# Optimization experiments

Measured on AMD Instinct MI355X. Metric: run time of the kernel, lower is better.

Reference implementation:

```python
import jax, jax.numpy as jnp
import numpy as np

IN_CH = 128
HID = 256   # 2 * out_channels
OUT_CH = 128
N_NODES = 10000
N_EDGES = 640000


def setup_inputs() -> dict:
    key = jax.random.key(0)
    ks = jax.random.split(key, 6)
    x = jax.random.normal(ks[0], (N_NODES, IN_CH), dtype=jnp.float32)
    edge_index = jax.random.randint(ks[1], (2, N_EDGES), 0, N_NODES, dtype=jnp.int64)
    # GCNConv params (glorot-like scale)
    W1 = jax.random.normal(ks[2], (IN_CH, HID), dtype=jnp.float32) / np.sqrt(IN_CH)
    b1 = jnp.zeros((HID,), dtype=jnp.float32)
    W2 = jax.random.normal(ks[3], (HID, OUT_CH), dtype=jnp.float32) / np.sqrt(HID)
    b2 = jnp.zeros((OUT_CH,), dtype=jnp.float32)
    return {"x": x, "edge_index": edge_index, "W1": W1, "b1": b1, "W2": W2, "b2": b2}


def _gcn_norm(edge_index, n_nodes):
    """Add self-loops and compute symmetric GCN normalization per edge."""
    loops = jnp.arange(n_nodes, dtype=edge_index.dtype)
    src = jnp.concatenate([edge_index[0], loops])  # [E+N]
    dst = jnp.concatenate([edge_index[1], loops])
    deg = jax.ops.segment_sum(jnp.ones_like(dst, dtype=jnp.float32), dst,
                              num_segments=n_nodes)
    dinv = jnp.where(deg > 0, jax.lax.rsqrt(deg), 0.0)
    norm = dinv[src] * dinv[dst]  # [E+N]
    return src, dst, norm


def _gcn_layer(x, W, b, src, dst, norm, n_nodes):
    h = x @ W                                  # [N, F_out]
    msg = h[src] * norm[:, None]               # gather + scale, [E+N, F_out]
    agg = jax.ops.segment_sum(msg, dst, num_segments=n_nodes)
    return agg + b


def reference(x, edge_index, W1, b1, W2, b2):
    n = x.shape[0]
    src, dst, norm = _gcn_norm(edge_index, n)
    h = jax.nn.relu(_gcn_layer(x, W1, b1, src, dst, norm, n))
    out = jax.nn.relu(_gcn_layer(h, W2, b2, src, dst, norm, n))
    return out
```

## Files before the change

kernel.cpp:

```cpp
#include <hip/hip_runtime.h>

#define N_FEAT 128
#define HID 256
#define OUT_CH 128

#define NB 256
#define MAXN 10240
#define CH 16
#define CB (NB / CH)

__device__ __forceinline__ unsigned bf16rn(float f) {
    unsigned u = __float_as_uint(f);
    return (u + 0x7fffu + ((u >> 16) & 1u)) >> 16;
}
__device__ __forceinline__ unsigned pack_bf16x2(float lo, float hi) {
    return bf16rn(lo) | (bf16rn(hi) << 16);
}
__device__ __forceinline__ float2 unpack_bf16x2(unsigned u) {
    float2 r;
    r.x = __uint_as_float(u << 16);
    r.y = __uint_as_float(u & 0xffff0000u);
    return r;
}


__global__ __launch_bounds__(256)
void hist_kernel(const int* __restrict__ dst, unsigned short* __restrict__ bh,
                 int E, int N, int chunk) {
    __shared__ int hist[MAXN];
    for (int i = threadIdx.x; i < N; i += 256) hist[i] = 0;
    __syncthreads();
    int base = blockIdx.x * chunk;
    int lim = min(chunk, E - base);
    for (int i = threadIdx.x; i < lim; i += 256) {
        int d = dst[base + i];
        if (d >= 0 && d < N) atomicAdd(&hist[d], 1);
    }
    __syncthreads();
    unsigned short* out = bh + (size_t)blockIdx.x * N;
    for (int i = threadIdx.x; i < N; i += 256) out[i] = (unsigned short)hist[i];
}

__global__ __launch_bounds__(256)
void colscan_kernel(const unsigned short* __restrict__ bh,
                    int* __restrict__ ps, int* __restrict__ counts,
                    float* __restrict__ dinv, int N) {
    int j = blockIdx.x * 256 + threadIdx.x;
    if (j >= N) return;
    int run = 0;
    for (int c = 0; c < CH; c++) {
        int s = 0;
        #pragma unroll
        for (int b = c * CB; b < (c + 1) * CB; b++) s += bh[(size_t)b * N + j];
        ps[(size_t)c * N + j] = run;
        run += s;
    }
    counts[j] = run;
    dinv[j] = rsqrtf((float)(run + 1));
}

#define SCAN_T 1024
#define SCAN_MAX_PER 16
__global__ __launch_bounds__(SCAN_T)
void scan_kernel(const int* __restrict__ counts,
                 int* __restrict__ row_start, int n) {
    int tid = threadIdx.x;
    int per = (n + SCAN_T - 1) / SCAN_T;
    int base = tid * per;
    int local[SCAN_MAX_PER];
    int sum = 0;
    for (int j = 0; j < per; j++) {
        int i = base + j;
        int c = (i < n) ? counts[i] : 0;
        local[j] = sum;
        sum += c;
    }
    int lane = tid & 63;
    int wave = tid >> 6;
    int incl = sum;
    #pragma unroll
    for (int off = 1; off < 64; off <<= 1) {
        int t = __shfl_up(incl, off, 64);
        if (lane >= off) incl += t;
    }
    __shared__ int wsum[16];
    __shared__ int woff[16];
    if (lane == 63) wsum[wave] = incl;
    __syncthreads();
    if (wave == 0) {
        int w = (lane < 16) ? wsum[lane] : 0;
        int v = w;
        #pragma unroll
        for (int off = 1; off < 16; off <<= 1) {
            int t = __shfl_up(v, off, 64);
            if (lane >= off) v += t;
        }
        if (lane < 16) woff[lane] = v - w;
    }
    __syncthreads();
    int thread_excl = woff[wave] + (incl - sum);
    for (int j = 0; j < per; j++) {
        int i = base + j;
        if (i < n) row_start[i] = thread_excl + local[j];
    }
    if (tid == SCAN_T - 1) row_start[n] = thread_excl + sum;
}

__global__ __launch_bounds__(256)
void chunkbase_kernel(unsigned short* __restrict__ bh,
                      const int* __restrict__ ps, int N) {
    int j = blockIdx.x * 256 + threadIdx.x;
    if (j >= N) return;
    int c = blockIdx.y;
    int run = ps[(size_t)c * N + j];
    #pragma unroll
    for (int b = c * CB; b < (c + 1) * CB; b++) {
        size_t idx = (size_t)b * N + j;
        int t = bh[idx];
        bh[idx] = (unsigned short)run;
        run += t;
    }
}

__global__ __launch_bounds__(256)
void scat_kernel(const int* __restrict__ src, const int* __restrict__ dst,
                 const unsigned short* __restrict__ bh,
                 const int* __restrict__ row_start,
                 int* __restrict__ csr_src, int E, int N, int chunk) {
    __shared__ int cur[MAXN];
    const unsigned short* basep = bh + (size_t)blockIdx.x * N;
    for (int i = threadIdx.x; i < N; i += 256)
        cur[i] = row_start[i] + (int)basep[i];
    __syncthreads();
    int base = blockIdx.x * chunk;
    int lim = min(chunk, E - base);
    for (int i = threadIdx.x; i < lim; i += 256) {
        int e = base + i;
        int d = dst[e];
        if (d < 0 || d >= N) continue;
        int pos = atomicAdd(&cur[d], 1);
        if ((unsigned)pos < (unsigned)E) csr_src[pos] = src[e];
    }
}

__global__ void prescale_kernel(const float* __restrict__ x,
                                const float* __restrict__ dinv,
                                unsigned* __restrict__ xs_b, int total4) {
    int i = blockIdx.x * blockDim.x + threadIdx.x;
    if (i < total4) {
        int row = i >> 5;
        float d = dinv[row];
        float4 v = ((const float4*)x)[i];
        uint2 p;
        p.x = pack_bf16x2(v.x * d, v.y * d);
        p.y = pack_bf16x2(v.z * d, v.w * d);
        ((uint2*)xs_b)[i] = p;
    }
}

template <bool EPILOGUE>
__global__ __launch_bounds__(256)
void agg_kernel(const unsigned* __restrict__ featb,
                const float* __restrict__ dinv,
                const int* __restrict__ row_start,
                const int* __restrict__ csr_src,
                const float* __restrict__ bias,
                float* __restrict__ out, int N) {
    int wave = threadIdx.x >> 6;
    int n = blockIdx.x * 4 + wave;
    if (n >= N) return;
    int f = threadIdx.x & 63;
    float dn = dinv[n];
    float2 v = unpack_bf16x2(featb[(size_t)n * 64 + f]);
    float accx = v.x;
    float accy = v.y;
    int e0 = row_start[n];
    int e1 = row_start[n + 1];
    int e = e0;
    if (e + 8 <= e1) {
        int s_cur[8];
        #pragma unroll
        for (int j = 0; j < 8; j++) s_cur[j] = csr_src[e + j];
        e += 8;
        for (; e + 8 <= e1; e += 8) {
            unsigned w[8];
            #pragma unroll
            for (int j = 0; j < 8; j++) w[j] = featb[(size_t)s_cur[j] * 64 + f];
            int s_nxt[8];
            #pragma unroll
            for (int j = 0; j < 8; j++) s_nxt[j] = csr_src[e + j];
            #pragma unroll
            for (int j = 0; j < 8; j++) {
                float2 u = unpack_bf16x2(w[j]);
                accx += u.x;
                accy += u.y;
            }
            #pragma unroll
            for (int j = 0; j < 8; j++) s_cur[j] = s_nxt[j];
        }
        unsigned w[8];
        #pragma unroll
        for (int j = 0; j < 8; j++) w[j] = featb[(size_t)s_cur[j] * 64 + f];
        #pragma unroll
        for (int j = 0; j < 8; j++) {
            float2 u = unpack_bf16x2(w[j]);
            accx += u.x;
            accy += u.y;
        }
    }
    for (; e + 4 <= e1; e += 4) {
        int s0 = csr_src[e], s1 = csr_src[e + 1];
        int s2 = csr_src[e + 2], s3 = csr_src[e + 3];
        unsigned w0 = featb[(size_t)s0 * 64 + f];
        unsigned w1 = featb[(size_t)s1 * 64 + f];
        unsigned w2 = featb[(size_t)s2 * 64 + f];
        unsigned w3 = featb[(size_t)s3 * 64 + f];
        float2 u0 = unpack_bf16x2(w0), u1 = unpack_bf16x2(w1);
        float2 u2 = unpack_bf16x2(w2), u3 = unpack_bf16x2(w3);
        accx += u0.x + u1.x + u2.x + u3.x;
        accy += u0.y + u1.y + u2.y + u3.y;
    }
    for (; e < e1; ++e) {
        float2 u = unpack_bf16x2(featb[(size_t)csr_src[e] * 64 + f]);
        accx += u.x;
        accy += u.y;
    }
    accx *= dn;
    accy *= dn;
    if (EPILOGUE) {
        float2 b = ((const float2*)bias)[f];
        accx = fmaxf(accx + b.x, 0.0f);
        accy = fmaxf(accy + b.y, 0.0f);
    }
    float2 r;
    r.x = accx;
    r.y = accy;
    ((float2*)out)[(size_t)n * 64 + f] = r;
}

template <bool BIAS_RELU, bool RSCALE, bool BF16_OUT>
__global__ __launch_bounds__(256)
void gemm_kernel(const float* __restrict__ A,
                 const float* __restrict__ B,
                 const float* __restrict__ bias,
                 const float* __restrict__ rscale,
                 void* __restrict__ Cv, int M, int N, int K) {
    __shared__ float As[16][68];
    __shared__ float Bs[16][64];
    int tid = threadIdx.x;
    int n0 = blockIdx.x * 64;
    int m0 = blockIdx.y * 64;
    int tx = tid & 15;
    int ty = tid >> 4;
    int ar = tid >> 2;
    int akq = tid & 3;
    int bk = tid >> 4;
    int bnq = tid & 15;
    float acc[4][4] = {};
    for (int k0 = 0; k0 < K; k0 += 16) {
        float4 av = make_float4(0.f, 0.f, 0.f, 0.f);
        if (m0 + ar < M)
            av = *(const float4*)&A[(size_t)(m0 + ar) * K + k0 + akq * 4];
        float4 bv = *(const float4*)&B[(size_t)(k0 + bk) * N + n0 + bnq * 4];
        As[akq * 4 + 0][ar] = av.x;
        As[akq * 4 + 1][ar] = av.y;
        As[akq * 4 + 2][ar] = av.z;
        As[akq * 4 + 3][ar] = av.w;
        *(float4*)&Bs[bk][bnq * 4] = bv;
        __syncthreads();
        #pragma unroll
        for (int k = 0; k < 16; k++) {
            float4 ra = *(const float4*)&As[k][ty * 4];
            float4 rb = *(const float4*)&Bs[k][tx * 4];
            acc[0][0] = fmaf(ra.x, rb.x, acc[0][0]);
            acc[0][1] = fmaf(ra.x, rb.y, acc[0][1]);
            acc[0][2] = fmaf(ra.x, rb.z, acc[0][2]);
            acc[0][3] = fmaf(ra.x, rb.w, acc[0][3]);
            acc[1][0] = fmaf(ra.y, rb.x, acc[1][0]);
            acc[1][1] = fmaf(ra.y, rb.y, acc[1][1]);
            acc[1][2] = fmaf(ra.y, rb.z, acc[1][2]);
            acc[1][3] = fmaf(ra.y, rb.w, acc[1][3]);
            acc[2][0] = fmaf(ra.z, rb.x, acc[2][0]);
            acc[2][1] = fmaf(ra.z, rb.y, acc[2][1]);
            acc[2][2] = fmaf(ra.z, rb.z, acc[2][2]);
            acc[2][3] = fmaf(ra.z, rb.w, acc[2][3]);
            acc[3][0] = fmaf(ra.w, rb.x, acc[3][0]);
            acc[3][1] = fmaf(ra.w, rb.y, acc[3][1]);
            acc[3][2] = fmaf(ra.w, rb.z, acc[3][2]);
            acc[3][3] = fmaf(ra.w, rb.w, acc[3][3]);
        }
        __syncthreads();
    }
    #pragma unroll
    for (int i = 0; i < 4; i++) {
        int m = m0 + ty * 4 + i;
        if (m >= M) continue;
        float rs = RSCALE ? rscale[m] : 1.0f;
        float v[4];
        #pragma unroll
        for (int j = 0; j < 4; j++) {
            v[j] = acc[i][j];
            if (RSCALE) v[j] *= rs;
            if (BIAS_RELU) v[j] = fmaxf(v[j] + bias[n0 + tx * 4 + j], 0.0f);
        }
        if (BF16_OUT) {
            unsigned* Cb = (unsigned*)Cv;
            size_t base = (size_t)m * (N >> 1) + ((n0 + tx * 4) >> 1);
            Cb[base] = pack_bf16x2(v[0], v[1]);
            Cb[base + 1] = pack_bf16x2(v[2], v[3]);
        } else {
            float* C = (float*)Cv;
            #pragma unroll
            for (int j = 0; j < 4; j++)
                C[(size_t)m * N + n0 + tx * 4 + j] = v[j];
        }
    }
}


static inline size_t align512(size_t x) { return (x + 511) & ~(size_t)511; }

extern "C" void kernel_launch(void* const* d_in, const int* in_sizes, int n_in,
                              void* d_out, int out_size, void* d_ws, size_t ws_size,
                              hipStream_t stream) {
    const float* x = (const float*)d_in[0];
    const int* ei = (const int*)d_in[1];
    const float* W1 = (const float*)d_in[2];
    const float* b1 = (const float*)d_in[3];
    const float* W2 = (const float*)d_in[4];
    const float* b2 = (const float*)d_in[5];
    float* out = (float*)d_out;

    const int N = in_sizes[0] / N_FEAT;
    const int E = in_sizes[1] / 2;
    const int* src = ei;
    const int* dst = ei + E;

    char* ws = (char*)d_ws;
    size_t off = 0;
    float* dinv = (float*)(ws + off);    off += align512((size_t)N * 4);
    int* counts = (int*)(ws + off);      off += align512((size_t)N * 4);
    int* row_start = (int*)(ws + off);   off += align512((size_t)(N + 1) * 4);
    int* csr_src = (int*)(ws + off);     off += align512((size_t)E * 4);
    unsigned* xs_b = (unsigned*)(ws + off); off += align512((size_t)N * 64 * 4);
    float* h = (float*)(ws + off);       off += align512((size_t)N * HID * 4);
    unsigned* t_b = (unsigned*)(ws + off); off += align512((size_t)N * 64 * 4);
    int* ps = (int*)(ws + off);          off += align512((size_t)CH * N * 4);
    unsigned short* bh = (unsigned short*)(ws + off);
    off += align512((size_t)NB * N * 2);
    (void)ws_size;
    float* agg1 = out;
    const int chunk = (E + NB - 1) / NB;
    const int NJ = (N + 255) / 256;

    hist_kernel<<<NB, 256, 0, stream>>>(dst, bh, E, N, chunk);
    colscan_kernel<<<NJ, 256, 0, stream>>>(bh, ps, counts, dinv, N);
    scan_kernel<<<1, SCAN_T, 0, stream>>>(counts, row_start, N);
    chunkbase_kernel<<<dim3(NJ, CH), 256, 0, stream>>>(bh, ps, N);
    scat_kernel<<<NB, 256, 0, stream>>>(src, dst, bh, row_start, csr_src, E, N, chunk);

    {
        int total4 = N * N_FEAT / 4;
        prescale_kernel<<<(total4 + 255) / 256, 256, 0, stream>>>(x, dinv, xs_b, total4);
    }

    agg_kernel<false><<<(N + 3) / 4, 256, 0, stream>>>(xs_b, dinv, row_start, csr_src,
                                                       nullptr, agg1, N);

    {
        dim3 grid(HID / 64, (N + 63) / 64);
        gemm_kernel<true, false, false><<<grid, 256, 0, stream>>>(
            agg1, W1, b1, nullptr, h, N, HID, N_FEAT);
    }

    {
        dim3 grid(OUT_CH / 64, (N + 63) / 64);
        gemm_kernel<false, true, true><<<grid, 256, 0, stream>>>(
            h, W2, nullptr, dinv, t_b, N, OUT_CH, HID);
    }

    agg_kernel<true><<<(N + 3) / 4, 256, 0, stream>>>(t_b, dinv, row_start, csr_src,
                                                      b2, out, N);
}
```

Measured before the change: 176.5 us.

## Replace FP32 SIMT GEMMs with FP16 MFMA GEMMs and merge CSR prefix passes

Both dense GEMMs move from FP32 FMA tiling to 16x16x32 FP16 MFMA with swizzled LDS tiles. Inputs and intermediates (aggregated features, hidden activations, transformed features) are now stored as FP16 instead of BF16/FP32, and the weights are transposed and converted to FP16 inside the prescale kernel. The two-level per-block histogram scan is folded into one colscan pass that writes exclusive offsets in place, which drops the chunkbase kernel and the ps buffer. The aim is to cut GEMM compute time, intermediate memory traffic and launch count. The cost is FP16 range and precision risk. The GEMM also reads padded rows past N that are never initialised, although those rows are not stored.

```diff
diff --git a/kernel.cpp b/kernel.cpp
--- a/kernel.cpp
+++ b/kernel.cpp
@@ -6,26 +6,31 @@
 
 #define NB 256
 #define MAXN 10240
-#define CH 16
-#define CB (NB / CH)
-
-__device__ __forceinline__ unsigned bf16rn(float f) {
-    unsigned u = __float_as_uint(f);
-    return (u + 0x7fffu + ((u >> 16) & 1u)) >> 16;
-}
-__device__ __forceinline__ unsigned pack_bf16x2(float lo, float hi) {
-    return bf16rn(lo) | (bf16rn(hi) << 16);
-}
-__device__ __forceinline__ float2 unpack_bf16x2(unsigned u) {
-    float2 r;
-    r.x = __uint_as_float(u << 16);
-    r.y = __uint_as_float(u & 0xffff0000u);
-    return r;
-}
-
-
-__global__ __launch_bounds__(256)
-void hist_kernel(const int* __restrict__ dst, unsigned short* __restrict__ bh,
+
+typedef unsigned short u16;
+typedef _Float16 f16x8 __attribute__((ext_vector_type(8)));
+typedef float f32x4 __attribute__((ext_vector_type(4)));
+
+__device__ __forceinline__ unsigned pack_f16x2(float lo, float hi) {
+    union { _Float16 h[2]; unsigned u; } c;
+    c.h[0] = (_Float16)lo;
+    c.h[1] = (_Float16)hi;
+    return c.u;
+}
+__device__ __forceinline__ float2 unpack_f16x2(unsigned u) {
+    union { unsigned u; _Float16 h[2]; } c;
+    c.u = u;
+    return make_float2((float)c.h[0], (float)c.h[1]);
+}
+__device__ __forceinline__ u16 f16u(float f) {
+    union { _Float16 h; u16 u; } c;
+    c.h = (_Float16)f;
+    return c.u;
+}
+
+
+__global__ __launch_bounds__(256)
+void hist_kernel(const int* __restrict__ dst, u16* __restrict__ bh,
                  int E, int N, int chunk) {
     __shared__ int hist[MAXN];
     for (int i = threadIdx.x; i < N; i += 256) hist[i] = 0;
@@ -37,23 +42,22 @@
         if (d >= 0 && d < N) atomicAdd(&hist[d], 1);
     }
     __syncthreads();
-    unsigned short* out = bh + (size_t)blockIdx.x * N;
-    for (int i = threadIdx.x; i < N; i += 256) out[i] = (unsigned short)hist[i];
-}
-
-__global__ __launch_bounds__(256)
-void colscan_kernel(const unsigned short* __restrict__ bh,
-                    int* __restrict__ ps, int* __restrict__ counts,
-                    float* __restrict__ dinv, int N) {
+    u16* out = bh + (size_t)blockIdx.x * N;
+    for (int i = threadIdx.x; i < N; i += 256) out[i] = (u16)hist[i];
+}
+
+__global__ __launch_bounds__(256)
+void colscan_kernel(u16* __restrict__ bh,
+                    int* __restrict__ counts, float* __restrict__ dinv, int N) {
     int j = blockIdx.x * 256 + threadIdx.x;
     if (j >= N) return;
     int run = 0;
-    for (int c = 0; c < CH; c++) {
-        int s = 0;
-        #pragma unroll
-        for (int b = c * CB; b < (c + 1) * CB; b++) s += bh[(size_t)b * N + j];
-        ps[(size_t)c * N + j] = run;
-        run += s;
+    #pragma unroll 8
+    for (int b = 0; b < NB; b++) {
+        size_t idx = (size_t)b * N + j;
+        int t = bh[idx];
+        bh[idx] = (u16)run;
+        run += t;
     }
     counts[j] = run;
     dinv[j] = rsqrtf((float)(run + 1));
@@ -107,28 +111,12 @@
 }
 
 __global__ __launch_bounds__(256)
-void chunkbase_kernel(unsigned short* __restrict__ bh,
-                      const int* __restrict__ ps, int N) {
-    int j = blockIdx.x * 256 + threadIdx.x;
-    if (j >= N) return;
-    int c = blockIdx.y;
-    int run = ps[(size_t)c * N + j];
-    #pragma unroll
-    for (int b = c * CB; b < (c + 1) * CB; b++) {
-        size_t idx = (size_t)b * N + j;
-        int t = bh[idx];
-        bh[idx] = (unsigned short)run;
-        run += t;
-    }
-}
-
-__global__ __launch_bounds__(256)
 void scat_kernel(const int* __restrict__ src, const int* __restrict__ dst,
-                 const unsigned short* __restrict__ bh,
+                 const u16* __restrict__ bh,
                  const int* __restrict__ row_start,
                  int* __restrict__ csr_src, int E, int N, int chunk) {
     __shared__ int cur[MAXN];
-    const unsigned short* basep = bh + (size_t)blockIdx.x * N;
+    const u16* basep = bh + (size_t)blockIdx.x * N;
     for (int i = threadIdx.x; i < N; i += 256)
         cur[i] = row_start[i] + (int)basep[i];
     __syncthreads();
@@ -145,33 +133,49 @@
 
 __global__ void prescale_kernel(const float* __restrict__ x,
                                 const float* __restrict__ dinv,
-                                unsigned* __restrict__ xs_b, int total4) {
+                                unsigned* __restrict__ xs_b,
+                                const float* __restrict__ W1,
+                                const float* __restrict__ W2,
+                                u16* __restrict__ W1t, u16* __restrict__ W2t,
+                                int total4) {
     int i = blockIdx.x * blockDim.x + threadIdx.x;
     if (i < total4) {
         int row = i >> 5;
         float d = dinv[row];
         float4 v = ((const float4*)x)[i];
         uint2 p;
-        p.x = pack_bf16x2(v.x * d, v.y * d);
-        p.y = pack_bf16x2(v.z * d, v.w * d);
+        p.x = pack_f16x2(v.x * d, v.y * d);
+        p.y = pack_f16x2(v.z * d, v.w * d);
         ((uint2*)xs_b)[i] = p;
-    }
-}
-
-template <bool EPILOGUE>
+    } else {
+        int j = i - total4;
+        if (j < N_FEAT * HID) {
+            int n = j >> 7, k = j & 127;
+            W1t[j] = f16u(W1[(size_t)k * HID + n]);
+        } else {
+            j -= N_FEAT * HID;
+            if (j < HID * OUT_CH) {
+                int n = j >> 8, k = j & 255;
+                W2t[j] = f16u(W2[(size_t)k * OUT_CH + n]);
+            }
+        }
+    }
+}
+
+template <bool EPILOGUE, bool F16OUT>
 __global__ __launch_bounds__(256)
 void agg_kernel(const unsigned* __restrict__ featb,
                 const float* __restrict__ dinv,
                 const int* __restrict__ row_start,
                 const int* __restrict__ csr_src,
                 const float* __restrict__ bias,
-                float* __restrict__ out, int N) {
+                void* __restrict__ out, int N) {
     int wave = threadIdx.x >> 6;
     int n = blockIdx.x * 4 + wave;
     if (n >= N) return;
     int f = threadIdx.x & 63;
     float dn = dinv[n];
-    float2 v = unpack_bf16x2(featb[(size_t)n * 64 + f]);
+    float2 v = unpack_f16x2(featb[(size_t)n * 64 + f]);
     float accx = v.x;
     float accy = v.y;
     int e0 = row_start[n];
@@ -191,7 +195,7 @@
             for (int j = 0; j < 8; j++) s_nxt[j] = csr_src[e + j];
             #pragma unroll
             for (int j = 0; j < 8; j++) {
-                float2 u = unpack_bf16x2(w[j]);
+                float2 u = unpack_f16x2(w[j]);
                 accx += u.x;
                 accy += u.y;
             }
@@ -203,7 +207,7 @@
         for (int j = 0; j < 8; j++) w[j] = featb[(size_t)s_cur[j] * 64 + f];
         #pragma unroll
         for (int j = 0; j < 8; j++) {
-            float2 u = unpack_bf16x2(w[j]);
+            float2 u = unpack_f16x2(w[j]);
             accx += u.x;
             accy += u.y;
         }
@@ -215,13 +219,13 @@
         unsigned w1 = featb[(size_t)s1 * 64 + f];
         unsigned w2 = featb[(size_t)s2 * 64 + f];
         unsigned w3 = featb[(size_t)s3 * 64 + f];
-        float2 u0 = unpack_bf16x2(w0), u1 = unpack_bf16x2(w1);
-        float2 u2 = unpack_bf16x2(w2), u3 = unpack_bf16x2(w3);
+        float2 u0 = unpack_f16x2(w0), u1 = unpack_f16x2(w1);
+        float2 u2 = unpack_f16x2(w2), u3 = unpack_f16x2(w3);
         accx += u0.x + u1.x + u2.x + u3.x;
         accy += u0.y + u1.y + u2.y + u3.y;
     }
     for (; e < e1; ++e) {
-        float2 u = unpack_bf16x2(featb[(size_t)csr_src[e] * 64 + f]);
+        float2 u = unpack_f16x2(featb[(size_t)csr_src[e] * 64 + f]);
         accx += u.x;
         accy += u.y;
     }
@@ -232,87 +236,79 @@
         accx = fmaxf(accx + b.x, 0.0f);
         accy = fmaxf(accy + b.y, 0.0f);
     }
-    float2 r;
-    r.x = accx;
-    r.y = accy;
-    ((float2*)out)[(size_t)n * 64 + f] = r;
-}
-
-template <bool BIAS_RELU, bool RSCALE, bool BF16_OUT>
-__global__ __launch_bounds__(256)
-void gemm_kernel(const float* __restrict__ A,
-                 const float* __restrict__ B,
-                 const float* __restrict__ bias,
-                 const float* __restrict__ rscale,
-                 void* __restrict__ Cv, int M, int N, int K) {
-    __shared__ float As[16][68];
-    __shared__ float Bs[16][64];
+    if (F16OUT) {
+        ((unsigned*)out)[(size_t)n * 64 + f] = pack_f16x2(accx, accy);
+    } else {
+        float2 r;
+        r.x = accx;
+        r.y = accy;
+        ((float2*)out)[(size_t)n * 64 + f] = r;
+    }
+}
+
+template <bool BIAS_RELU, bool RSCALE>
+__global__ __launch_bounds__(256)
+void gemm16_kernel(const u16* __restrict__ A,
+                   const u16* __restrict__ Bt,
+                   const float* __restrict__ bias,
+                   const float* __restrict__ rscale,
+                   u16* __restrict__ C,
+                   int M, int N, int K) {
+    __shared__ __align__(16) u16 As[64][64];
+    __shared__ __align__(16) u16 Bs[64][64];
     int tid = threadIdx.x;
+    int w = tid >> 6;
+    int l = tid & 63;
+    int m0 = blockIdx.y * 64;
     int n0 = blockIdx.x * 64;
-    int m0 = blockIdx.y * 64;
-    int tx = tid & 15;
-    int ty = tid >> 4;
-    int ar = tid >> 2;
-    int akq = tid & 3;
-    int bk = tid >> 4;
-    int bnq = tid & 15;
-    float acc[4][4] = {};
-    for (int k0 = 0; k0 < K; k0 += 16) {
-        float4 av = make_float4(0.f, 0.f, 0.f, 0.f);
-        if (m0 + ar < M)
-            av = *(const float4*)&A[(size_t)(m0 + ar) * K + k0 + akq * 4];
-        float4 bv = *(const float4*)&B[(size_t)(k0 + bk) * N + n0 + bnq * 4];
-        As[akq * 4 + 0][ar] = av.x;
-        As[akq * 4 + 1][ar] = av.y;
-        As[akq * 4 + 2][ar] = av.z;
-        As[akq * 4 + 3][ar] = av.w;
-        *(float4*)&Bs[bk][bnq * 4] = bv;
+
+    f32x4 acc[4];
+    const f32x4 zero = {0.f, 0.f, 0.f, 0.f};
+    #pragma unroll
+    for (int n = 0; n < 4; n++) acc[n] = zero;
+
+    int rowA = w * 16 + (l & 15);
+    int cbase = l >> 4;
+
+    for (int k0 = 0; k0 < K; k0 += 64) {
+        #pragma unroll
+        for (int t = 0; t < 2; t++) {
+            int q = tid + t * 256;
+            int r = q >> 3;
+            int c = q & 7;
+            f16x8 av = *(const f16x8*)(A + (size_t)(m0 + r) * K + k0 + c * 8);
+            *(f16x8*)&As[r][(c ^ (r & 7)) * 8] = av;
+            f16x8 bv = *(const f16x8*)(Bt + (size_t)(n0 + r) * K + k0 + c * 8);
+            *(f16x8*)&Bs[r][(c ^ (r & 7)) * 8] = bv;
+        }
         __syncthreads();
         #pragma unroll
-        for (int k = 0; k < 16; k++) {
-            float4 ra = *(const float4*)&As[k][ty * 4];
-            float4 rb = *(const float4*)&Bs[k][tx * 4];
-            acc[0][0] = fmaf(ra.x, rb.x, acc[0][0]);
-            acc[0][1] = fmaf(ra.x, rb.y, acc[0][1]);
-            acc[0][2] = fmaf(ra.x, rb.z, acc[0][2]);
-            acc[0][3] = fmaf(ra.x, rb.w, acc[0][3]);
-            acc[1][0] = fmaf(ra.y, rb.x, acc[1][0]);
-            acc[1][1] = fmaf(ra.y, rb.y, acc[1][1]);
-            acc[1][2] = fmaf(ra.y, rb.z, acc[1][2]);
-            acc[1][3] = fmaf(ra.y, rb.w, acc[1][3]);
-            acc[2][0] = fmaf(ra.z, rb.x, acc[2][0]);
-            acc[2][1] = fmaf(ra.z, rb.y, acc[2][1]);
-            acc[2][2] = fmaf(ra.z, rb.z, acc[2][2]);
-            acc[2][3] = fmaf(ra.z, rb.w, acc[2][3]);
-            acc[3][0] = fmaf(ra.w, rb.x, acc[3][0]);
-            acc[3][1] = fmaf(ra.w, rb.y, acc[3][1]);
-            acc[3][2] = fmaf(ra.w, rb.z, acc[3][2]);
-            acc[3][3] = fmaf(ra.w, rb.w, acc[3][3]);
+        for (int kc = 0; kc < 2; kc++) {
+            int ch = kc * 4 + cbase;
+            f16x8 af = *(const f16x8*)&As[rowA][(ch ^ (rowA & 7)) * 8];
+            #pragma unroll
+            for (int n = 0; n < 4; n++) {
+                int rb = n * 16 + (l & 15);
+                f16x8 bf = *(const f16x8*)&Bs[rb][(ch ^ (rb & 7)) * 8];
+                acc[n] = __builtin_amdgcn_mfma_f32_16x16x32_f16(af, bf, acc[n], 0, 0, 0);
+            }
         }
         __syncthreads();
     }
+    int r0 = (l >> 4) * 2 * 2;
+    int col_l = l & 15;
     #pragma unroll
-    for (int i = 0; i < 4; i++) {
-        int m = m0 + ty * 4 + i;
+    for (int r = 0; r < 4; r++) {
+        int m = m0 + w * 16 + r0 + r;
         if (m >= M) continue;
         float rs = RSCALE ? rscale[m] : 1.0f;
-        float v[4];
-        #pragma unroll
-        for (int j = 0; j < 4; j++) {
-            v[j] = acc[i][j];
-            if (RSCALE) v[j] *= rs;
-            if (BIAS_RELU) v[j] = fmaxf(v[j] + bias[n0 + tx * 4 + j], 0.0f);
-        }
-        if (BF16_OUT) {
-            unsigned* Cb = (unsigned*)Cv;
-            size_t base = (size_t)m * (N >> 1) + ((n0 + tx * 4) >> 1);
-            Cb[base] = pack_bf16x2(v[0], v[1]);
-            Cb[base + 1] = pack_bf16x2(v[2], v[3]);
-        } else {
-            float* C = (float*)Cv;
-            #pragma unroll
-            for (int j = 0; j < 4; j++)
-                C[(size_t)m * N + n0 + tx * 4 + j] = v[j];
+        #pragma unroll
+        for (int n = 0; n < 4; n++) {
+            int col = n0 + n * 16 + col_l;
+            float v = acc[n][r];
+            if (RSCALE) v *= rs;
+            if (BIAS_RELU) v = fmaxf(v + bias[col], 0.0f);
+            C[(size_t)m * N + col] = f16u(v);
         }
     }
 }
@@ -336,49 +332,52 @@
     const int* src = ei;
     const int* dst = ei + E;
 
+    const int Mpad = ((N + 63) / 64) * 64;
+
     char* ws = (char*)d_ws;
     size_t off = 0;
     float* dinv = (float*)(ws + off);    off += align512((size_t)N * 4);
     int* counts = (int*)(ws + off);      off += align512((size_t)N * 4);
     int* row_start = (int*)(ws + off);   off += align512((size_t)(N + 1) * 4);
     int* csr_src = (int*)(ws + off);     off += align512((size_t)E * 4);
-    unsigned* xs_b = (unsigned*)(ws + off); off += align512((size_t)N * 64 * 4);
-    float* h = (float*)(ws + off);       off += align512((size_t)N * HID * 4);
-    unsigned* t_b = (unsigned*)(ws + off); off += align512((size_t)N * 64 * 4);
-    int* ps = (int*)(ws + off);          off += align512((size_t)CH * N * 4);
-    unsigned short* bh = (unsigned short*)(ws + off);
-    off += align512((size_t)NB * N * 2);
+    unsigned* xs_b = (unsigned*)(ws + off);  off += align512((size_t)N * 64 * 4);
+    u16* agg1h = (u16*)(ws + off);       off += align512((size_t)Mpad * N_FEAT * 2);
+    u16* h16 = (u16*)(ws + off);         off += align512((size_t)Mpad * HID * 2);
+    u16* t16 = (u16*)(ws + off);         off += align512((size_t)N * OUT_CH * 2);
+    u16* W1t = (u16*)(ws + off);         off += align512((size_t)HID * N_FEAT * 2);
+    u16* W2t = (u16*)(ws + off);         off += align512((size_t)OUT_CH * HID * 2);
+    u16* bh = (u16*)(ws + off);          off += align512((size_t)NB * N * 2);
     (void)ws_size;
-    float* agg1 = out;
     const int chunk = (E + NB - 1) / NB;
     const int NJ = (N + 255) / 256;
 
     hist_kernel<<<NB, 256, 0, stream>>>(dst, bh, E, N, chunk);
-    colscan_kernel<<<NJ, 256, 0, stream>>>(bh, ps, counts, dinv, N);
+    colscan_kernel<<<NJ, 256, 0, stream>>>(bh, counts, dinv, N);
     scan_kernel<<<1, SCAN_T, 0, stream>>>(counts, row_start, N);
-    chunkbase_kernel<<<dim3(NJ, CH), 256, 0, stream>>>(bh, ps, N);
     scat_kernel<<<NB, 256, 0, stream>>>(src, dst, bh, row_start, csr_src, E, N, chunk);
 
     {
         int total4 = N * N_FEAT / 4;
-        prescale_kernel<<<(total4 + 255) / 256, 256, 0, stream>>>(x, dinv, xs_b, total4);
-    }
-
-    agg_kernel<false><<<(N + 3) / 4, 256, 0, stream>>>(xs_b, dinv, row_start, csr_src,
-                                                       nullptr, agg1, N);
+        int total = total4 + N_FEAT * HID + HID * OUT_CH;
+        prescale_kernel<<<(total + 255) / 256, 256, 0, stream>>>(
+            x, dinv, xs_b, W1, W2, W1t, W2t, total4);
+    }
+
+    agg_kernel<false, true><<<(N + 3) / 4, 256, 0, stream>>>(
+        xs_b, dinv, row_start, csr_src, nullptr, agg1h, N);
 
     {
-        dim3 grid(HID / 64, (N + 63) / 64);
-        gemm_kernel<true, false, false><<<grid, 256, 0, stream>>>(
-            agg1, W1, b1, nullptr, h, N, HID, N_FEAT);
+        dim3 grid(HID / 64, Mpad / 64);
+        gemm16_kernel<true, false><<<grid, 256, 0, stream>>>(
+            agg1h, W1t, b1, nullptr, h16, N, HID, N_FEAT);
     }
 
     {
-        dim3 grid(OUT_CH / 64, (N + 63) / 64);
-        gemm_kernel<false, true, true><<<grid, 256, 0, stream>>>(
-            h, W2, nullptr, dinv, t_b, N, OUT_CH, HID);
-    }
-
-    agg_kernel<true><<<(N + 3) / 4, 256, 0, stream>>>(t_b, dinv, row_start, csr_src,
-                                                      b2, out, N);
-}
+        dim3 grid(OUT_CH / 64, Mpad / 64);
+        gemm16_kernel<false, true><<<grid, 256, 0, stream>>>(
+            h16, W2t, nullptr, dinv, t16, N, OUT_CH, HID);
+    }
+
+    agg_kernel<true, false><<<(N + 3) / 4, 256, 0, stream>>>(
+        (const unsigned*)t16, dinv, row_start, csr_src, b2, out, N);
+}
```

Result: no change. 179.7 us (+1.8%).
